# Performance work log

Measured on AMD Instinct MI355X. Metric: run time of the kernel, lower is better.

## Reference

```python
import jax, jax.numpy as jnp
import numpy as np

N_NODES = 50000
N_EDGES = 800000
D_IN = 128
HIDDEN = 128
N_LAYERS = 3
N_CLASSES = 10
N_GRAPHS = 512
BN_EPS = 1e-5


def gcn_conv(x, edges, W, b):
    """PyG GCNConv: D^{-1/2}(A+I)D^{-1/2} X W + b (self-loops added)."""
    N = x.shape[0]
    src, dst = edges[0], edges[1]
    # degrees with self-loops
    deg = jax.ops.segment_sum(jnp.ones(src.shape[0], x.dtype), dst, num_segments=N) + 1.0
    dinv = jax.lax.rsqrt(deg)
    h = x @ W                                   # [N, out]
    norm = dinv[src] * dinv[dst]                # [E]
    out = jax.ops.segment_sum(h[src] * norm[:, None], dst, num_segments=N)
    out = out + h * (dinv * dinv)[:, None]      # self-loop messages
    return out + b


def batch_norm(x, gamma, beta):
    # BatchNorm1d in training mode: batch stats over node axis, biased var
    mu = x.mean(axis=0)
    var = x.var(axis=0)
    return gamma * (x - mu) * jax.lax.rsqrt(var + BN_EPS) + beta


def setup_inputs() -> dict:
    key = jax.random.key(0)
    ks = jax.random.split(key, 12)
    x = jax.random.normal(ks[0], (N_NODES, D_IN), dtype=jnp.float32)
    edges = jax.random.randint(ks[1], (2, N_EDGES), 0, N_NODES, dtype=jnp.int64)
    batch = jnp.sort(jax.random.randint(ks[2], (N_NODES,), 0, N_GRAPHS, dtype=jnp.int64))
    s_in = 1.0 / np.sqrt(D_IN)
    s_h = 1.0 / np.sqrt(HIDDEN)
    return {
        "x": x,
        "edges": edges,
        "batch": batch,
        "W1": jax.random.normal(ks[3], (D_IN, HIDDEN), dtype=jnp.float32) * s_in,
        "b1": jnp.zeros((HIDDEN,), jnp.float32),
        "g1": jnp.ones((HIDDEN,), jnp.float32),
        "be1": jnp.zeros((HIDDEN,), jnp.float32),
        "Wc": jax.random.normal(ks[4], (N_LAYERS, HIDDEN, HIDDEN), dtype=jnp.float32) * s_h,
        "bc": jnp.zeros((N_LAYERS, HIDDEN), jnp.float32),
        "gc": jnp.ones((N_LAYERS, HIDDEN), jnp.float32),
        "bec": jnp.zeros((N_LAYERS, HIDDEN), jnp.float32),
        "Wl": jax.random.normal(ks[5], (HIDDEN, N_CLASSES), dtype=jnp.float32) * s_h,
        "bl": jnp.zeros((N_CLASSES,), jnp.float32),
    }


def reference(x, edges, batch, W1, b1, g1, be1, Wc, bc, gc, bec, Wl, bl):
    h = jax.nn.relu(batch_norm(gcn_conv(x, edges, W1, b1), g1, be1))
    for i in range(N_LAYERS):  # fixed small layer loop
        h = jax.nn.relu(batch_norm(gcn_conv(h, edges, Wc[i], bc[i]), gc[i], bec[i]))
    # global_mean_pool over per-node graph ids
    sums = jax.ops.segment_sum(h, batch, num_segments=N_GRAPHS)
    counts = jax.ops.segment_sum(jnp.ones(h.shape[0], h.dtype), batch, num_segments=N_GRAPHS)
    pooled = sums / jnp.maximum(counts, 1.0)[:, None]
    return pooled @ Wl + bl
```

## Files before the change

### kernel.cpp

```cpp
#include <hip/hip_runtime.h>
#include <hip/hip_bf16.h>

#define NN 50000
#define NE 800000
#define DH 128
#define NGRAPH 512
#define NCLS 10
#define BN_EPS 1e-5f
#define SCAN_NB ((NN + 255) / 256)
#define GEMM_NB ((NN + 63) / 64)
#define BN1_NB 1024
#define BN2_NB 32
#define FILL_SEG 392
#define FILL_NB (FILL_SEG * 8)
#define STRIPE ((NN + 7) / 8)

typedef unsigned int uint;
typedef unsigned short ushort;
typedef __attribute__((ext_vector_type(8))) short short8;
typedef __attribute__((ext_vector_type(4))) float f32x4;

__device__ __forceinline__ ushort f2bf(float x) {
    __hip_bfloat16 h = __float2bfloat16(x);
    return *(ushort*)&h;
}


__global__ void hist_kernel(const int* __restrict__ dst, int* __restrict__ counts, int E) {
    int e = blockIdx.x * blockDim.x + threadIdx.x;
    if (e < E) atomicAdd(&counts[dst[e]], 1);
}

__global__ void compute_dinv_kernel(const int* __restrict__ counts, float* __restrict__ dinv, int N) {
    int n = blockIdx.x * blockDim.x + threadIdx.x;
    if (n < N) dinv[n] = rsqrtf((float)(counts[n] + 1));
}

__launch_bounds__(256)
__global__ void scan1_kernel(const int* __restrict__ counts, int* __restrict__ bsum, int N) {
    __shared__ int ls[256];
    int i = blockIdx.x * 256 + threadIdx.x;
    ls[threadIdx.x] = (i < N) ? counts[i] : 0;
    __syncthreads();
    for (int off = 128; off > 0; off >>= 1) {
        if (threadIdx.x < off) ls[threadIdx.x] += ls[threadIdx.x + off];
        __syncthreads();
    }
    if (threadIdx.x == 0) bsum[blockIdx.x] = ls[0];
}

__launch_bounds__(256)
__global__ void scan2_kernel(int* __restrict__ bsum, int NB) {
    __shared__ int ls[256];
    int tid = threadIdx.x;
    int v = (tid < NB) ? bsum[tid] : 0;
    ls[tid] = v;
    __syncthreads();
    for (int off = 1; off < 256; off <<= 1) {
        int t = (tid >= off) ? ls[tid - off] : 0;
        __syncthreads();
        ls[tid] += t;
        __syncthreads();
    }
    if (tid < NB) bsum[tid] = ls[tid] - v;
}

__launch_bounds__(256)
__global__ void scan3_kernel(const int* __restrict__ counts, const int* __restrict__ boff,
                             int* __restrict__ offsets, int* __restrict__ cursor, int N) {
    __shared__ int ls[256];
    int tid = threadIdx.x;
    int i = blockIdx.x * 256 + tid;
    int v = (i < N) ? counts[i] : 0;
    ls[tid] = v;
    __syncthreads();
    for (int off = 1; off < 256; off <<= 1) {
        int t = (tid >= off) ? ls[tid - off] : 0;
        __syncthreads();
        ls[tid] += t;
        __syncthreads();
    }
    int base = boff[blockIdx.x];
    if (i < N) {
        int ex = base + ls[tid] - v;
        offsets[i] = ex;
        cursor[i] = ex;
        if (i == N - 1) offsets[N] = base + ls[tid];
    }
}

__launch_bounds__(256)
__global__ void fill_kernel(const int* __restrict__ src, const int* __restrict__ dst,
                            int* __restrict__ cursor, int* __restrict__ csr_src, int E) {
    int stripe = blockIdx.x & 7;
    int seg = blockIdx.x >> 3;
    int lo = stripe * STRIPE;
    int hi = lo + STRIPE;
    for (int e = seg * 256 + threadIdx.x; e < E; e += FILL_SEG * 256) {
        int d = dst[e];
        if (d >= lo && d < hi) {
            int pos = atomicAdd(&cursor[d], 1);
            csr_src[pos] = src[e];
        }
    }
}


__launch_bounds__(256)
__global__ void wtrans_kernel(const float* __restrict__ W1, const float* __restrict__ Wc,
                              ushort* __restrict__ WT) {
    int layer = blockIdx.x >> 4;
    int kt = (blockIdx.x >> 2) & 3, nt = blockIdx.x & 3;
    const float* W = (layer == 0) ? W1 : Wc + (size_t)(layer - 1) * DH * DH;
    __shared__ float tile[32][33];
    int t = threadIdx.x;
    int r = t >> 3;
    int c4 = (t & 7) * 4;
    float4 v = *(const float4*)&W[(size_t)(kt * 32 + r) * DH + nt * 32 + c4];
    tile[r][c4 + 0] = v.x; tile[r][c4 + 1] = v.y;
    tile[r][c4 + 2] = v.z; tile[r][c4 + 3] = v.w;
    __syncthreads();
    int n = t >> 3, k4 = (t & 7) * 4;
    ushort4 o;
    o.x = f2bf(tile[k4 + 0][n]);
    o.y = f2bf(tile[k4 + 1][n]);
    o.z = f2bf(tile[k4 + 2][n]);
    o.w = f2bf(tile[k4 + 3][n]);
    *(ushort4*)&WT[(size_t)layer * DH * DH + (size_t)(nt * 32 + n) * DH + kt * 32 + k4] = o;
}


template<int MODE>
__launch_bounds__(256)
__global__ void gemm_kernel(const float* __restrict__ X, const ushort* __restrict__ WTl,
                            const float* __restrict__ bnacc, const float* __restrict__ gamma,
                            const float* __restrict__ beta, const float* __restrict__ dinv,
                            ushort* __restrict__ H, int N) {
    __shared__ uint4 xs4[64 * 16];
    __shared__ uint4 wt4[128 * 16];
    int t = threadIdx.x;
    int kc = t & 15;
    int row0 = blockIdx.x * 64;

    float sc[8], sh[8];
    if (MODE) {
        const float invN = 1.0f / (float)NN;
        #pragma unroll
        for (int j = 0; j < 8; j++) {
            int f = kc * 8 + j;
            float mean = bnacc[f] * invN;
            float var = bnacc[128 + f] * invN - mean * mean;
            float s = gamma[f] * rsqrtf(var + BN_EPS);
            sc[j] = s;
            sh[j] = beta[f] - mean * s;
        }
    }

    const float4* X4 = (const float4*)X;
    #pragma unroll
    for (int i = 0; i < 4; i++) {
        int row = (t >> 4) + i * 16;
        int r = row0 + row;
        float v[8];
        if (r < N) {
            float4 a = X4[(size_t)r * 32 + kc * 2];
            float4 b = X4[(size_t)r * 32 + kc * 2 + 1];
            v[0] = a.x; v[1] = a.y; v[2] = a.z; v[3] = a.w;
            v[4] = b.x; v[5] = b.y; v[6] = b.z; v[7] = b.w;
            if (MODE) {
                #pragma unroll
                for (int j = 0; j < 8; j++) v[j] = fmaxf(v[j] * sc[j] + sh[j], 0.f);
            }
        } else {
            #pragma unroll
            for (int j = 0; j < 8; j++) v[j] = 0.f;
        }
        uint4 p;
        p.x = (uint)f2bf(v[0]) | ((uint)f2bf(v[1]) << 16);
        p.y = (uint)f2bf(v[2]) | ((uint)f2bf(v[3]) << 16);
        p.z = (uint)f2bf(v[4]) | ((uint)f2bf(v[5]) << 16);
        p.w = (uint)f2bf(v[6]) | ((uint)f2bf(v[7]) << 16);
        xs4[row * 16 + (kc ^ (row & 7))] = p;
    }
    const uint4* WT4 = (const uint4*)WTl;
    #pragma unroll
    for (int i = 0; i < 8; i++) {
        int n = (t >> 4) + i * 16;
        wt4[n * 16 + (kc ^ (n & 7))] = WT4[n * 16 + kc];
    }
    __syncthreads();

    int w = t >> 6, l = t & 63;
    int l16 = l >> 4;
    int lrow = w * 16 + (l & 15);
    f32x4 acc[8];
    #pragma unroll
    for (int c = 0; c < 8; c++) acc[c] = (f32x4){0.f, 0.f, 0.f, 0.f};

    #pragma unroll
    for (int ks = 0; ks < 4; ks++) {
        int kk = ks * 4 + l16;
        uint4 av = xs4[lrow * 16 + (kk ^ (lrow & 7))];
        short8 a = *(short8*)&av;
        #pragma unroll
        for (int c = 0; c < 8; c++) {
            int n = c * 16 + (l & 15);
            uint4 bv = wt4[n * 16 + (kk ^ (n & 7))];
            short8 b = *(short8*)&bv;
            acc[c] = __builtin_amdgcn_mfma_f32_16x16x32_bf16(a, b, acc[c], 0, 0, 0);
        }
    }

    #pragma unroll
    for (int j = 0; j < 4; j++) {
        int grow = row0 + w * 16 + l16 * 4 + j;
        if (grow < N) {
            float dv = dinv[grow];
            #pragma unroll
            for (int c = 0; c < 8; c++) {
                H[(size_t)grow * DH + c * 16 + (l & 15)] = f2bf(acc[c][j] * dv);
            }
        }
    }
}


__device__ __forceinline__ float bf_lo(uint v) { return __uint_as_float(v << 16); }
__device__ __forceinline__ float bf_hi(uint v) { return __uint_as_float(v & 0xffff0000u); }

__launch_bounds__(256)
__global__ void agg_kernel(const uint* __restrict__ H, const int* __restrict__ offsets,
                           const int* __restrict__ csr_src, const float* __restrict__ dinv,
                           const float* __restrict__ bias, float* __restrict__ out, int N) {
    int n = blockIdx.x * 4 + (threadIdx.x >> 6);
    int lane = threadIdx.x & 63;
    if (n >= N) return;
    int beg = offsets[n], end = offsets[n + 1];
    float ax = 0.f, ay = 0.f;
    int e = beg;
    for (; e + 7 < end; e += 8) {
        int s0 = csr_src[e];
        int s1 = csr_src[e + 1];
        int s2 = csr_src[e + 2];
        int s3 = csr_src[e + 3];
        int s4 = csr_src[e + 4];
        int s5 = csr_src[e + 5];
        int s6 = csr_src[e + 6];
        int s7 = csr_src[e + 7];
        uint v0 = H[(size_t)s0 * 64 + lane];
        uint v1 = H[(size_t)s1 * 64 + lane];
        uint v2 = H[(size_t)s2 * 64 + lane];
        uint v3 = H[(size_t)s3 * 64 + lane];
        uint v4 = H[(size_t)s4 * 64 + lane];
        uint v5 = H[(size_t)s5 * 64 + lane];
        uint v6 = H[(size_t)s6 * 64 + lane];
        uint v7 = H[(size_t)s7 * 64 + lane];
        ax += bf_lo(v0) + bf_lo(v1) + bf_lo(v2) + bf_lo(v3)
            + bf_lo(v4) + bf_lo(v5) + bf_lo(v6) + bf_lo(v7);
        ay += bf_hi(v0) + bf_hi(v1) + bf_hi(v2) + bf_hi(v3)
            + bf_hi(v4) + bf_hi(v5) + bf_hi(v6) + bf_hi(v7);
    }
    for (; e < end; e++) {
        uint v = H[(size_t)csr_src[e] * 64 + lane];
        ax += bf_lo(v);
        ay += bf_hi(v);
    }
    uint vn = H[(size_t)n * 64 + lane];
    ax += bf_lo(vn);
    ay += bf_hi(vn);
    float dv = dinv[n];
    float2 b = ((const float2*)bias)[lane];
    ((float2*)out)[(size_t)n * 64 + lane] = make_float2(ax * dv + b.x, ay * dv + b.y);
}


__launch_bounds__(256)
__global__ void bnstats1_kernel(const float* __restrict__ A, float* __restrict__ part, int N) {
    int f = threadIdx.x & 127;
    int rh = threadIdx.x >> 7;
    float s = 0.f, sq = 0.f;
    for (int r = blockIdx.x * 2 + rh; r < N; r += BN1_NB * 2) {
        float v = A[(size_t)r * DH + f];
        s += v;
        sq += v * v;
    }
    __shared__ float ls[256], lq[256];
    ls[threadIdx.x] = s;
    lq[threadIdx.x] = sq;
    __syncthreads();
    if (threadIdx.x < 128) {
        part[(size_t)blockIdx.x * 256 + threadIdx.x] = ls[threadIdx.x] + ls[threadIdx.x + 128];
        part[(size_t)blockIdx.x * 256 + 128 + threadIdx.x] = lq[threadIdx.x] + lq[threadIdx.x + 128];
    }
}

__launch_bounds__(256)
__global__ void bnstats2_kernel(const float* __restrict__ part, float* __restrict__ acc) {
    int rows = BN1_NB / BN2_NB;
    float s = 0.f;
    int r0 = blockIdx.x * rows;
    for (int r = r0; r < r0 + rows; r++) s += part[(size_t)r * 256 + threadIdx.x];
    atomicAdd(&acc[threadIdx.x], s);
}


__device__ __forceinline__ int lower_bound_dev(const int* __restrict__ a, int n, int key) {
    int lo = 0, hi = n;
    while (lo < hi) {
        int m = (lo + hi) >> 1;
        if (a[m] < key) lo = m + 1; else hi = m;
    }
    return lo;
}

__launch_bounds__(256)
__global__ void pool_kernel(const float* __restrict__ AGG, const int* __restrict__ batch,
                            const float* __restrict__ bnacc, const float* __restrict__ gamma,
                            const float* __restrict__ beta, float* __restrict__ pooled, int N) {
    int g = blockIdx.x;
    __shared__ int sbeg, send;
    if (threadIdx.x == 0) {
        sbeg = lower_bound_dev(batch, N, g);
        send = lower_bound_dev(batch, N, g + 1);
    }
    __syncthreads();
    int beg = sbeg, end = send;
    int f = threadIdx.x & 127;
    int rh = threadIdx.x >> 7;
    const float invN = 1.0f / (float)NN;
    float mean = bnacc[f] * invN;
    float var = bnacc[128 + f] * invN - mean * mean;
    float sc = gamma[f] * rsqrtf(var + BN_EPS);
    float shf = beta[f] - mean * sc;
    float s = 0.f;
    for (int r = beg + rh; r < end; r += 2)
        s += fmaxf(AGG[(size_t)r * DH + f] * sc + shf, 0.f);
    __shared__ float ls[256];
    ls[threadIdx.x] = s;
    __syncthreads();
    if (threadIdx.x < 128) {
        float tot = ls[threadIdx.x] + ls[threadIdx.x + 128];
        float cnt = (float)(end - beg);
        pooled[g * DH + f] = tot / fmaxf(cnt, 1.f);
    }
}


__launch_bounds__(256)
__global__ void final_kernel(const float* __restrict__ pooled, const float* __restrict__ Wl,
                             const float* __restrict__ bl, float* __restrict__ out) {
    int gid = blockIdx.x * blockDim.x + threadIdx.x;
    if (gid >= NGRAPH * NCLS) return;
    int g = gid / NCLS, c = gid % NCLS;
    float s = bl[c];
    #pragma unroll 8
    for (int k = 0; k < DH; k++) s += pooled[g * DH + k] * Wl[k * NCLS + c];
    out[gid] = s;
}


extern "C" void kernel_launch(void* const* d_in, const int* in_sizes, int n_in,
                              void* d_out, int out_size, void* d_ws, size_t ws_size,
                              hipStream_t stream) {
    const float* x     = (const float*)d_in[0];
    const int*   edges = (const int*)d_in[1];
    const int*   batch = (const int*)d_in[2];
    const float* W1    = (const float*)d_in[3];
    const float* b1    = (const float*)d_in[4];
    const float* g1    = (const float*)d_in[5];
    const float* be1   = (const float*)d_in[6];
    const float* Wc    = (const float*)d_in[7];
    const float* bc    = (const float*)d_in[8];
    const float* gc    = (const float*)d_in[9];
    const float* bec   = (const float*)d_in[10];
    const float* Wl    = (const float*)d_in[11];
    const float* bl    = (const float*)d_in[12];
    float* out = (float*)d_out;

    const int* esrc = edges;
    const int* edst = edges + NE;

    char* w = (char*)d_ws;
    auto alloc = [&](size_t bytes) -> void* {
        void* p = (void*)w;
        w += (bytes + 255) & ~(size_t)255;
        return p;
    };
    int*    counts  = (int*)alloc(NN * 4);
    int*    offsets = (int*)alloc((NN + 1) * 4);
    int*    cursor  = (int*)alloc(NN * 4);
    float*  dinv    = (float*)alloc(NN * 4);
    int*    csr_src = (int*)alloc(NE * 4);
    int*    bsum    = (int*)alloc(256 * 4);
    float*  bn_acc  = (float*)alloc(4 * 256 * 4);
    float*  bn_part = (float*)alloc((size_t)BN1_NB * 256 * 4);
    float*  pooled  = (float*)alloc(NGRAPH * DH * 4);
    ushort* WT      = (ushort*)alloc(4 * DH * DH * 2);
    uint*   H       = (uint*)alloc((size_t)NN * 64 * 4);
    float*  AGG     = (float*)alloc((size_t)NN * DH * 4);

    hipMemsetAsync(counts, 0, NN * 4, stream);
    hipMemsetAsync(bn_acc, 0, 4 * 256 * 4, stream);
    hist_kernel<<<(NE + 255) / 256, 256, 0, stream>>>(edst, counts, NE);
    compute_dinv_kernel<<<(NN + 255) / 256, 256, 0, stream>>>(counts, dinv, NN);
    scan1_kernel<<<SCAN_NB, 256, 0, stream>>>(counts, bsum, NN);
    scan2_kernel<<<1, 256, 0, stream>>>(bsum, SCAN_NB);
    scan3_kernel<<<SCAN_NB, 256, 0, stream>>>(counts, bsum, offsets, cursor, NN);
    fill_kernel<<<FILL_NB, 256, 0, stream>>>(esrc, edst, cursor, csr_src, NE);
    wtrans_kernel<<<64, 256, 0, stream>>>(W1, Wc, WT);

    const float* act = x;
    for (int l = 0; l < 4; l++) {
        const float* bm  = (l == 0) ? b1 : bc + (size_t)(l - 1) * DH;
        const float* gp  = (l == 1) ? g1 : gc + (size_t)(l - 2) * DH;
        const float* bep = (l == 1) ? be1 : bec + (size_t)(l - 2) * DH;
        const ushort* WTl = WT + (size_t)l * DH * DH;

        if (l == 0) {
            gemm_kernel<0><<<GEMM_NB, 256, 0, stream>>>(
                act, WTl, nullptr, nullptr, nullptr, dinv, (ushort*)H, NN);
        } else {
            gemm_kernel<1><<<GEMM_NB, 256, 0, stream>>>(
                act, WTl, bn_acc + (size_t)(l - 1) * 256, gp, bep, dinv, (ushort*)H, NN);
        }
        agg_kernel<<<(NN + 3) / 4, 256, 0, stream>>>(H, offsets, csr_src, dinv, bm, AGG, NN);
        bnstats1_kernel<<<BN1_NB, 256, 0, stream>>>(AGG, bn_part, NN);
        bnstats2_kernel<<<BN2_NB, 256, 0, stream>>>(bn_part, bn_acc + (size_t)l * 256);
        act = AGG;
    }

    pool_kernel<<<NGRAPH, 256, 0, stream>>>(AGG, batch, bn_acc + 3 * 256,
                                            gc + 2 * DH, bec + 2 * DH, pooled, NN);
    final_kernel<<<(NGRAPH * NCLS + 255) / 256, 256, 0, stream>>>(pooled, Wl, bl, out);
}
```

Before: 383.0 us.

## Store aggregated activations as bf16 and predicate the gather loop

The aggregation output buffer changes from fp32 to packed bf16 pairs, and the GEMM, BN-stats and pooling kernels now read that packed format. This halves the bytes written and read for the intermediate activations in every layer. The gather loop also drops its scalar remainder loop in favour of a predicated 8-wide batch, reading a small padding past the end of csr_src. BN statistics are now computed from bf16-rounded values, which adds some precision loss.

```diff
diff --git a/kernel.cpp b/kernel.cpp
--- a/kernel.cpp
+++ b/kernel.cpp
@@ -24,6 +24,8 @@
     __hip_bfloat16 h = __float2bfloat16(x);
     return *(ushort*)&h;
 }
+__device__ __forceinline__ float bf_lo(uint v) { return __uint_as_float(v << 16); }
+__device__ __forceinline__ float bf_hi(uint v) { return __uint_as_float(v & 0xffff0000u); }
 
 
 __global__ void hist_kernel(const int* __restrict__ dst, int* __restrict__ counts, int E) {
@@ -132,7 +134,8 @@
 
 template<int MODE>
 __launch_bounds__(256)
-__global__ void gemm_kernel(const float* __restrict__ X, const ushort* __restrict__ WTl,
+__global__ void gemm_kernel(const float* __restrict__ Xf, const uint* __restrict__ Xb,
+                            const ushort* __restrict__ WTl,
                             const float* __restrict__ bnacc, const float* __restrict__ gamma,
                             const float* __restrict__ beta, const float* __restrict__ dinv,
                             ushort* __restrict__ H, int N) {
@@ -156,20 +159,25 @@
         }
     }
 
-    const float4* X4 = (const float4*)X;
     #pragma unroll
     for (int i = 0; i < 4; i++) {
         int row = (t >> 4) + i * 16;
         int r = row0 + row;
         float v[8];
         if (r < N) {
-            float4 a = X4[(size_t)r * 32 + kc * 2];
-            float4 b = X4[(size_t)r * 32 + kc * 2 + 1];
-            v[0] = a.x; v[1] = a.y; v[2] = a.z; v[3] = a.w;
-            v[4] = b.x; v[5] = b.y; v[6] = b.z; v[7] = b.w;
             if (MODE) {
+                uint4 raw = ((const uint4*)Xb)[(size_t)r * 16 + kc];
+                v[0] = bf_lo(raw.x); v[1] = bf_hi(raw.x);
+                v[2] = bf_lo(raw.y); v[3] = bf_hi(raw.y);
+                v[4] = bf_lo(raw.z); v[5] = bf_hi(raw.z);
+                v[6] = bf_lo(raw.w); v[7] = bf_hi(raw.w);
                 #pragma unroll
                 for (int j = 0; j < 8; j++) v[j] = fmaxf(v[j] * sc[j] + sh[j], 0.f);
+            } else {
+                float4 a = ((const float4*)Xf)[(size_t)r * 32 + kc * 2];
+                float4 b = ((const float4*)Xf)[(size_t)r * 32 + kc * 2 + 1];
+                v[0] = a.x; v[1] = a.y; v[2] = a.z; v[3] = a.w;
+                v[4] = b.x; v[5] = b.y; v[6] = b.z; v[7] = b.w;
             }
         } else {
             #pragma unroll
@@ -225,72 +233,63 @@
 }
 
 
-__device__ __forceinline__ float bf_lo(uint v) { return __uint_as_float(v << 16); }
-__device__ __forceinline__ float bf_hi(uint v) { return __uint_as_float(v & 0xffff0000u); }
-
 __launch_bounds__(256)
 __global__ void agg_kernel(const uint* __restrict__ H, const int* __restrict__ offsets,
                            const int* __restrict__ csr_src, const float* __restrict__ dinv,
-                           const float* __restrict__ bias, float* __restrict__ out, int N) {
+                           const float* __restrict__ bias, uint* __restrict__ out, int N) {
     int n = blockIdx.x * 4 + (threadIdx.x >> 6);
     int lane = threadIdx.x & 63;
     if (n >= N) return;
     int beg = offsets[n], end = offsets[n + 1];
     float ax = 0.f, ay = 0.f;
-    int e = beg;
-    for (; e + 7 < end; e += 8) {
-        int s0 = csr_src[e];
-        int s1 = csr_src[e + 1];
-        int s2 = csr_src[e + 2];
-        int s3 = csr_src[e + 3];
-        int s4 = csr_src[e + 4];
-        int s5 = csr_src[e + 5];
-        int s6 = csr_src[e + 6];
-        int s7 = csr_src[e + 7];
-        uint v0 = H[(size_t)s0 * 64 + lane];
-        uint v1 = H[(size_t)s1 * 64 + lane];
-        uint v2 = H[(size_t)s2 * 64 + lane];
-        uint v3 = H[(size_t)s3 * 64 + lane];
-        uint v4 = H[(size_t)s4 * 64 + lane];
-        uint v5 = H[(size_t)s5 * 64 + lane];
-        uint v6 = H[(size_t)s6 * 64 + lane];
-        uint v7 = H[(size_t)s7 * 64 + lane];
-        ax += bf_lo(v0) + bf_lo(v1) + bf_lo(v2) + bf_lo(v3)
-            + bf_lo(v4) + bf_lo(v5) + bf_lo(v6) + bf_lo(v7);
-        ay += bf_hi(v0) + bf_hi(v1) + bf_hi(v2) + bf_hi(v3)
-            + bf_hi(v4) + bf_hi(v5) + bf_hi(v6) + bf_hi(v7);
-    }
-    for (; e < end; e++) {
-        uint v = H[(size_t)csr_src[e] * 64 + lane];
-        ax += bf_lo(v);
-        ay += bf_hi(v);
+    for (int e = beg; e < end; e += 8) {
+        uint v[8];
+        #pragma unroll
+        for (int i = 0; i < 8; i++) {
+            int ee = e + i;
+            int sraw = csr_src[ee];
+            int s = (ee < end) ? sraw : n;
+            v[i] = H[(size_t)s * 64 + lane];
+        }
+        #pragma unroll
+        for (int i = 0; i < 8; i++) {
+            uint vv = (e + i < end) ? v[i] : 0u;
+            ax += bf_lo(vv);
+            ay += bf_hi(vv);
+        }
     }
     uint vn = H[(size_t)n * 64 + lane];
     ax += bf_lo(vn);
     ay += bf_hi(vn);
     float dv = dinv[n];
     float2 b = ((const float2*)bias)[lane];
-    ((float2*)out)[(size_t)n * 64 + lane] = make_float2(ax * dv + b.x, ay * dv + b.y);
-}
-
-
-__launch_bounds__(256)
-__global__ void bnstats1_kernel(const float* __restrict__ A, float* __restrict__ part, int N) {
-    int f = threadIdx.x & 127;
-    int rh = threadIdx.x >> 7;
-    float s = 0.f, sq = 0.f;
-    for (int r = blockIdx.x * 2 + rh; r < N; r += BN1_NB * 2) {
-        float v = A[(size_t)r * DH + f];
-        s += v;
-        sq += v * v;
-    }
-    __shared__ float ls[256], lq[256];
-    ls[threadIdx.x] = s;
-    lq[threadIdx.x] = sq;
-    __syncthreads();
-    if (threadIdx.x < 128) {
-        part[(size_t)blockIdx.x * 256 + threadIdx.x] = ls[threadIdx.x] + ls[threadIdx.x + 128];
-        part[(size_t)blockIdx.x * 256 + 128 + threadIdx.x] = lq[threadIdx.x] + lq[threadIdx.x + 128];
+    float ox = ax * dv + b.x;
+    float oy = ay * dv + b.y;
+    out[(size_t)n * 64 + lane] = (uint)f2bf(ox) | ((uint)f2bf(oy) << 16);
+}
+
+
+__launch_bounds__(256)
+__global__ void bnstats1_kernel(const uint* __restrict__ A, float* __restrict__ part, int N) {
+    int u = threadIdx.x & 63;
+    int rh = threadIdx.x >> 6;
+    float slo = 0.f, shi = 0.f, qlo = 0.f, qhi = 0.f;
+    for (int r = blockIdx.x * 4 + rh; r < N; r += BN1_NB * 4) {
+        uint v = A[(size_t)r * 64 + u];
+        float lo = bf_lo(v), hi = bf_hi(v);
+        slo += lo; shi += hi;
+        qlo += lo * lo; qhi += hi * hi;
+    }
+    __shared__ float4 red[4][64];
+    red[rh][u] = make_float4(slo, shi, qlo, qhi);
+    __syncthreads();
+    if (threadIdx.x < 64) {
+        float4 a = red[0][u], b = red[1][u], c = red[2][u], d = red[3][u];
+        float* p = part + (size_t)blockIdx.x * 256;
+        p[2 * u]           = a.x + b.x + c.x + d.x;
+        p[2 * u + 1]       = a.y + b.y + c.y + d.y;
+        p[128 + 2 * u]     = a.z + b.z + c.z + d.z;
+        p[128 + 2 * u + 1] = a.w + b.w + c.w + d.w;
     }
 }
 
@@ -314,7 +313,7 @@
 }
 
 __launch_bounds__(256)
-__global__ void pool_kernel(const float* __restrict__ AGG, const int* __restrict__ batch,
+__global__ void pool_kernel(const uint* __restrict__ AGG, const int* __restrict__ batch,
                             const float* __restrict__ bnacc, const float* __restrict__ gamma,
                             const float* __restrict__ beta, float* __restrict__ pooled, int N) {
     int g = blockIdx.x;
@@ -325,23 +324,30 @@
     }
     __syncthreads();
     int beg = sbeg, end = send;
-    int f = threadIdx.x & 127;
-    int rh = threadIdx.x >> 7;
+    int u = threadIdx.x & 63;
+    int rh = threadIdx.x >> 6;
     const float invN = 1.0f / (float)NN;
-    float mean = bnacc[f] * invN;
-    float var = bnacc[128 + f] * invN - mean * mean;
-    float sc = gamma[f] * rsqrtf(var + BN_EPS);
-    float shf = beta[f] - mean * sc;
-    float s = 0.f;
-    for (int r = beg + rh; r < end; r += 2)
-        s += fmaxf(AGG[(size_t)r * DH + f] * sc + shf, 0.f);
-    __shared__ float ls[256];
-    ls[threadIdx.x] = s;
-    __syncthreads();
-    if (threadIdx.x < 128) {
-        float tot = ls[threadIdx.x] + ls[threadIdx.x + 128];
-        float cnt = (float)(end - beg);
-        pooled[g * DH + f] = tot / fmaxf(cnt, 1.f);
+    float m0 = bnacc[2 * u] * invN,     m1 = bnacc[2 * u + 1] * invN;
+    float v0 = bnacc[128 + 2 * u] * invN - m0 * m0;
+    float v1 = bnacc[128 + 2 * u + 1] * invN - m1 * m1;
+    float sc0 = gamma[2 * u] * rsqrtf(v0 + BN_EPS);
+    float sc1 = gamma[2 * u + 1] * rsqrtf(v1 + BN_EPS);
+    float sh0 = beta[2 * u] - m0 * sc0;
+    float sh1 = beta[2 * u + 1] - m1 * sc1;
+    float s0 = 0.f, s1 = 0.f;
+    for (int r = beg + rh; r < end; r += 4) {
+        uint v = AGG[(size_t)r * 64 + u];
+        s0 += fmaxf(bf_lo(v) * sc0 + sh0, 0.f);
+        s1 += fmaxf(bf_hi(v) * sc1 + sh1, 0.f);
+    }
+    __shared__ float2 ls[4][64];
+    ls[rh][u] = make_float2(s0, s1);
+    __syncthreads();
+    if (threadIdx.x < 64) {
+        float2 a = ls[0][u], b = ls[1][u], c = ls[2][u], d = ls[3][u];
+        float cnt = fmaxf((float)(end - beg), 1.f);
+        pooled[g * DH + 2 * u]     = (a.x + b.x + c.x + d.x) / cnt;
+        pooled[g * DH + 2 * u + 1] = (a.y + b.y + c.y + d.y) / cnt;
     }
 }
 
@@ -390,14 +396,14 @@
     int*    offsets = (int*)alloc((NN + 1) * 4);
     int*    cursor  = (int*)alloc(NN * 4);
     float*  dinv    = (float*)alloc(NN * 4);
-    int*    csr_src = (int*)alloc(NE * 4);
+    int*    csr_src = (int*)alloc(NE * 4 + 64);
     int*    bsum    = (int*)alloc(256 * 4);
     float*  bn_acc  = (float*)alloc(4 * 256 * 4);
     float*  bn_part = (float*)alloc((size_t)BN1_NB * 256 * 4);
     float*  pooled  = (float*)alloc(NGRAPH * DH * 4);
     ushort* WT      = (ushort*)alloc(4 * DH * DH * 2);
     uint*   H       = (uint*)alloc((size_t)NN * 64 * 4);
-    float*  AGG     = (float*)alloc((size_t)NN * DH * 4);
+    uint*   AGG     = (uint*)alloc((size_t)NN * 64 * 4);
 
     hipMemsetAsync(counts, 0, NN * 4, stream);
     hipMemsetAsync(bn_acc, 0, 4 * 256 * 4, stream);
@@ -409,7 +415,6 @@
     fill_kernel<<<FILL_NB, 256, 0, stream>>>(esrc, edst, cursor, csr_src, NE);
     wtrans_kernel<<<64, 256, 0, stream>>>(W1, Wc, WT);
 
-    const float* act = x;
     for (int l = 0; l < 4; l++) {
         const float* bm  = (l == 0) ? b1 : bc + (size_t)(l - 1) * DH;
         const float* gp  = (l == 1) ? g1 : gc + (size_t)(l - 2) * DH;
@@ -418,15 +423,15 @@
 
         if (l == 0) {
             gemm_kernel<0><<<GEMM_NB, 256, 0, stream>>>(
-                act, WTl, nullptr, nullptr, nullptr, dinv, (ushort*)H, NN);
+                x, nullptr, WTl, nullptr, nullptr, nullptr, dinv, (ushort*)H, NN);
         } else {
             gemm_kernel<1><<<GEMM_NB, 256, 0, stream>>>(
-                act, WTl, bn_acc + (size_t)(l - 1) * 256, gp, bep, dinv, (ushort*)H, NN);
+                nullptr, AGG, WTl, bn_acc + (size_t)(l - 1) * 256, gp, bep, dinv,
+                (ushort*)H, NN);
         }
         agg_kernel<<<(NN + 3) / 4, 256, 0, stream>>>(H, offsets, csr_src, dinv, bm, AGG, NN);
         bnstats1_kernel<<<BN1_NB, 256, 0, stream>>>(AGG, bn_part, NN);
         bnstats2_kernel<<<BN2_NB, 256, 0, stream>>>(bn_part, bn_acc + (size_t)l * 256);
-        act = AGG;
     }
 
     pool_kernel<<<NGRAPH, 256, 0, stream>>>(AGG, batch, bn_acc + 3 * 256,
```

Result: faster. 325.1 us (-15.1%).
